# Performance work log

Measured on AMD Instinct MI355X. Metric: run time of the kernel, lower is better.

## Reference

```python
import jax, jax.numpy as jnp
import numpy as np

D = 1024
H = 4
HD = D // H
B = 256
L = 64
DILATIONS = (1, 4, 8, 16)


def setup_inputs() -> dict:
    key = jax.random.key(0)
    ks = jax.random.split(key, 12)
    s = 1.0 / np.sqrt(D)
    return {
        "x": jax.random.normal(ks[0], (B, D), jnp.float32),
        "hist": jax.random.normal(ks[1], (L, B, D), jnp.float32),
        "Wq": jax.random.normal(ks[2], (D, D), jnp.float32) * s,
        "bq": jnp.zeros((D,), jnp.float32),
        "Wk": jax.random.normal(ks[3], (D, D), jnp.float32) * s,
        "bk": jnp.zeros((D,), jnp.float32),
        "Wv": jax.random.normal(ks[4], (D, D), jnp.float32) * s,
        "bv": jnp.zeros((D,), jnp.float32),
        "Wo": jax.random.normal(ks[5], (D, D), jnp.float32) * s,
        "bo": jnp.zeros((D,), jnp.float32),
        "dil_w": jnp.full((len(DILATIONS),), 1.0 / len(DILATIONS), jnp.float32),
        "gamma": jnp.ones((D,), jnp.float32),
        "beta": jnp.zeros((D,), jnp.float32),
    }


def reference(x, hist, Wq, bq, Wk, bk, Wv, bv, Wo, bo, dil_w, gamma, beta):
    scale = 1.0 / np.sqrt(HD)
    q = (x @ Wq + bq).reshape(B, H, HD)  # (B, H, HD)
    attended = []
    for d in DILATIONS:
        # history frames at stride d, concatenated along dim 0 (faithful to torch.cat)
        frames = hist[::d].reshape(-1, D)              # (T', D), T' = ceil(L/d)*B
        k = (frames @ Wk + bk).reshape(-1, H, HD)      # (T', H, HD)
        v = (frames @ Wv + bv).reshape(-1, H, HD)
        s = jnp.einsum('bhd,thd->bht', q, k) * scale   # (B, H, T')
        a = jax.nn.softmax(s, axis=-1)
        attended.append(jnp.einsum('bht,thd->bhd', a, v).reshape(B, D))
    w = jax.nn.softmax(dil_w, axis=0)
    combined = sum(w[i] * attended[i] for i in range(len(DILATIONS)))
    y = x + combined @ Wo + bo
    mu = jnp.mean(y, axis=-1, keepdims=True)
    var = jnp.var(y, axis=-1, keepdims=True)
    return (y - mu) / jnp.sqrt(var + 1e-5) * gamma + beta
```

## Files before the change

kernel.cpp:

```cpp
#include <hip/hip_runtime.h>


#define DD    1024
#define TALL  16384

typedef _Float16 half8  __attribute__((ext_vector_type(8)));
typedef _Float16 half4v __attribute__((ext_vector_type(4)));
typedef float    floatx4 __attribute__((ext_vector_type(4)));
typedef unsigned int u32;

static const size_t OFF_WOT  = 0;
static const size_t OFF_WV16 = 2097152;
static const size_t OFF_WK16 = 4194304;
static const size_t OFF_WQ16 = 6291456;
static const size_t OFF_XB   = 8388608;
static const size_t OFF_G    = 8912896;
static const size_t OFF_WVOT = 11010048;
static const size_t OFF_WQKT = 19398656;
static const size_t OFF_BVWO = 27787264;
static const size_t OFF_BQK  = 27791360;
static const size_t OFF_PHR  = 27807744;
static const size_t OFF_OPP  = 29904896;
static const size_t OFF_HB   = 38293504;
static const size_t OFF_PHP  = OFF_HB;
static const size_t OFF_HT   = 71848960;
static const size_t OFF_S    = 105403392;

__device__ __forceinline__ void gl_lds16(const void* g, void* l) {
  __builtin_amdgcn_global_load_lds((const __attribute__((address_space(1))) u32*)g,
                                   (__attribute__((address_space(3))) u32*)l, 16, 0, 0);
}

__global__ void prep_kernel(const float* __restrict__ Wo, const float* __restrict__ Wv,
                            const float* __restrict__ Wk, const float* __restrict__ Wq,
                            const float* __restrict__ x, const float* __restrict__ hist,
                            _Float16* __restrict__ WoT, _Float16* __restrict__ Wv16,
                            _Float16* __restrict__ Wk16, _Float16* __restrict__ Wq16,
                            _Float16* __restrict__ xb, _Float16* __restrict__ histb,
                            _Float16* __restrict__ histT) {
  int bid = blockIdx.x, tid = threadIdx.x;
  if (bid < 1024) {
    int k0 = (bid & 31) * 32, n0 = (bid >> 5) * 32;
    __shared__ float t32[32][33];
    int tx = tid & 31, ty = tid >> 5;
#pragma unroll
    for (int i = 0; i < 4; i++) {
      int r = ty + i * 8;
      t32[r][tx] = Wo[(size_t)(k0 + r) * DD + n0 + tx];
    }
    __syncthreads();
#pragma unroll
    for (int i = 0; i < 4; i++) {
      int r = ty + i * 8;
      WoT[(size_t)(n0 + r) * DD + k0 + tx] = (_Float16)t32[tx][r];
    }
  } else if (bid < 4352) {
    const float* src; _Float16* dst; size_t i;
    if (bid < 2048)      { src = Wv; dst = Wv16; i = (size_t)(bid - 1024) * 256 + tid; }
    else if (bid < 3072) { src = Wk; dst = Wk16; i = (size_t)(bid - 2048) * 256 + tid; }
    else if (bid < 4096) { src = Wq; dst = Wq16; i = (size_t)(bid - 3072) * 256 + tid; }
    else                 { src = x;  dst = xb;   i = (size_t)(bid - 4096) * 256 + tid; }
    float4 v = ((const float4*)src)[i];
    half4v h = {(_Float16)v.x, (_Float16)v.y, (_Float16)v.z, (_Float16)v.w};
    *(half4v*)(dst + 4 * i) = h;
  } else {
    int tb = bid - 4352;
    int t0 = (tb & 255) * 64, f0 = (tb >> 8) * 64;
    __shared__ _Float16 lt[64][72];
    int r = tid >> 2, c0 = (tid & 3) * 16;
    half8 s0, s1;
#pragma unroll
    for (int i = 0; i < 4; i++) {
      float4 v = *(const float4*)&hist[(size_t)(t0 + r) * 1024 + f0 + c0 + i * 4];
      half4v h = {(_Float16)v.x, (_Float16)v.y, (_Float16)v.z, (_Float16)v.w};
      *(half4v*)&lt[r][c0 + i * 4] = h;
      if (i < 2) { s0[i*4]=h[0]; s0[i*4+1]=h[1]; s0[i*4+2]=h[2]; s0[i*4+3]=h[3]; }
      else { s1[(i-2)*4]=h[0]; s1[(i-2)*4+1]=h[1]; s1[(i-2)*4+2]=h[2]; s1[(i-2)*4+3]=h[3]; }
    }
    *(half8*)&histb[(size_t)(t0 + r) * 1024 + f0 + c0] = s0;
    *(half8*)&histb[(size_t)(t0 + r) * 1024 + f0 + c0 + 8] = s1;
    __syncthreads();
    int fr = tid >> 2, tc0 = (tid & 3) * 16;
    half8 o0, o1;
#pragma unroll
    for (int j = 0; j < 8; j++) { o0[j] = lt[tc0 + j][fr]; o1[j] = lt[tc0 + 8 + j][fr]; }
    *(half8*)&histT[(size_t)(f0 + fr) * TALL + t0 + tc0] = o0;
    *(half8*)&histT[(size_t)(f0 + fr) * TALL + t0 + tc0 + 8] = o1;
  }
}

__device__ __forceinline__ void gemm_core(const _Float16* __restrict__ A, size_t lda,
                                          const _Float16* __restrict__ B, size_t ldb,
                                          int kIters, _Float16* As, _Float16* Bs,
                                          int tid, floatx4 acc[4][4]) {
  int lane = tid & 63, w = tid >> 6;
  int l15 = lane & 15, quad = lane >> 4;
  int wm = (w >> 1) * 64, wn = (w & 1) * 64;
  int swz = ((tid & 3) ^ ((tid >> 3) & 3)) * 8;
  int pch = (quad ^ ((l15 >> 1) & 3)) * 8;
  const char* gA0 = (const char*)(A + (size_t)(tid >> 2) * lda + swz);
  const char* gA1 = (const char*)(A + ((size_t)(tid >> 2) + 64) * lda + swz);
  const char* gB0 = (const char*)(B + (size_t)(tid >> 2) * ldb + swz);
  const char* gB1 = (const char*)(B + ((size_t)(tid >> 2) + 64) * ldb + swz);
  _Float16* lA0 = As + w * 512; _Float16* lA1 = As + 2048 + w * 512;
  _Float16* lB0 = Bs + w * 512; _Float16* lB1 = Bs + 2048 + w * 512;
  for (int kk = 0; kk < kIters; kk++) {
    __syncthreads();
    size_t off = (size_t)kk * 64;
    gl_lds16(gA0 + off, lA0);
    gl_lds16(gA1 + off, lA1);
    gl_lds16(gB0 + off, lB0);
    gl_lds16(gB1 + off, lB1);
    __syncthreads();
    half8 a[4];
#pragma unroll
    for (int mi = 0; mi < 4; mi++) a[mi] = *(const half8*)&As[(wm + mi * 16 + l15) * 32 + pch];
#pragma unroll
    for (int ni = 0; ni < 4; ni++) {
      half8 b8 = *(const half8*)&Bs[(wn + ni * 16 + l15) * 32 + pch];
#pragma unroll
      for (int mi = 0; mi < 4; mi++)
        acc[mi][ni] = __builtin_amdgcn_mfma_f32_16x16x32_f16(a[mi], b8, acc[mi][ni], 0, 0, 0);
    }
  }
}

template <bool OUTF32>
__launch_bounds__(256, 3)
__global__ void gemm_f16_kernel(const _Float16* __restrict__ A, size_t lda, size_t aoffz,
                                const _Float16* __restrict__ B, size_t ldb, size_t boffz,
                                int kIters, const float* __restrict__ bias, size_t biasoffz,
                                float scale, void* __restrict__ C, size_t ldc, size_t coffz) {
  __shared__ __align__(16) _Float16 As[4096];
  __shared__ __align__(16) _Float16 Bs[4096];
  int tid = threadIdx.x;
  const _Float16* Ab = A + aoffz * blockIdx.z + (size_t)(blockIdx.y * 128) * lda;
  const _Float16* Bb = B + boffz * blockIdx.z + (size_t)(blockIdx.x * 128) * ldb;
  floatx4 acc[4][4];
  floatx4 zero = {0.f, 0.f, 0.f, 0.f};
#pragma unroll
  for (int a = 0; a < 4; a++)
#pragma unroll
    for (int b = 0; b < 4; b++) acc[a][b] = zero;
  gemm_core(Ab, lda, Bb, ldb, kIters, As, Bs, tid, acc);
  int lane = tid & 63, w = tid >> 6;
  int l15 = lane & 15, quad = lane >> 4;
  int wm = (w >> 1) * 64, wn = (w & 1) * 64;
#pragma unroll
  for (int mi = 0; mi < 4; mi++)
#pragma unroll
    for (int ni = 0; ni < 4; ni++) {
      int colg = blockIdx.x * 128 + wn + ni * 16 + l15;
      float bv = bias ? bias[biasoffz * blockIdx.z + colg] : 0.f;
#pragma unroll
      for (int r = 0; r < 4; r++) {
        int rowg = blockIdx.y * 128 + wm + mi * 16 + quad * 4 + r;
        float v = (acc[mi][ni][r] + bv) * scale;
        size_t idx = coffz * blockIdx.z + (size_t)rowg * ldc + colg;
        if (OUTF32) ((float*)C)[idx] = v;
        else ((_Float16*)C)[idx] = (_Float16)v;
      }
    }
}

__launch_bounds__(256, 3)
__global__ void wpack_kernel(const _Float16* __restrict__ WoT, const _Float16* __restrict__ Wv16,
                             const _Float16* __restrict__ Wk16, const _Float16* __restrict__ Wq16,
                             const float* __restrict__ bv, const float* __restrict__ bq,
                             _Float16* __restrict__ WVOT, _Float16* __restrict__ WQKT,
                             float* __restrict__ bvwo, float* __restrict__ bqk) {
  __shared__ __align__(16) _Float16 As[4096];
  __shared__ __align__(16) _Float16 Bs[4096];
  int bid = blockIdx.x, tid = threadIdx.x;
  if (bid < 512) {
    bool isQK = bid >= 256;
    int g = bid & 255;
    int x = g & 7, y = (g >> 3) & 7, z = g >> 6;
    const _Float16* A = isQK ? Wk16 : WoT;
    const _Float16* B = isQK ? Wq16 : Wv16;
    const _Float16* Ab = A + 256 * z + (size_t)(y * 128) * 1024;
    const _Float16* Bb = B + 256 * z + (size_t)(x * 128) * 1024;
    floatx4 acc[4][4];
    floatx4 zero = {0.f, 0.f, 0.f, 0.f};
#pragma unroll
    for (int a = 0; a < 4; a++)
#pragma unroll
      for (int b = 0; b < 4; b++) acc[a][b] = zero;
    gemm_core(Ab, 1024, Bb, 1024, 8, As, Bs, tid, acc);
    float scale = isQK ? 0.0625f : 1.0f;
    _Float16* C = isQK ? WQKT : WVOT;
    size_t ldc = isQK ? 1024 : 4096;
    size_t zoff = isQK ? (size_t)1048576 * z : (size_t)1024 * z;
    int lane = tid & 63, w = tid >> 6;
    int l15 = lane & 15, quad = lane >> 4;
    int wm = (w >> 1) * 64, wn = (w & 1) * 64;
#pragma unroll
    for (int mi = 0; mi < 4; mi++)
#pragma unroll
      for (int ni = 0; ni < 4; ni++) {
        int col = x * 128 + wn + ni * 16 + l15;
#pragma unroll
        for (int r = 0; r < 4; r++) {
          int row = y * 128 + wm + mi * 16 + quad * 4 + r;
          C[zoff + (size_t)row * ldc + col] = (_Float16)(acc[mi][ni][r] * scale);
        }
      }
  } else if (bid < 516) {
    int j = (bid - 512) * 256 + tid;
    const half8* row = (const half8*)(WoT + (size_t)j * 1024);
    float a = 0.f;
    for (int c = 0; c < 128; c++) {
      half8 w8 = row[c];
#pragma unroll
      for (int e = 0; e < 8; e++) a += bv[c * 8 + e] * (float)w8[e];
    }
    bvwo[j] = a;
  } else {
    int idx = (bid - 516) * 256 + tid;
    int h = idx >> 10, f = idx & 1023;
    const _Float16* row = Wk16 + (size_t)f * 1024 + h * 256;
    float a = 0.f;
    for (int n = 0; n < 256; n++) a += bq[h * 256 + n] * (float)row[n];
    bqk[idx] = a * 0.0625f;
  }
}

__launch_bounds__(256, 3)
__global__ void gemm_s_kernel(const _Float16* __restrict__ G, const _Float16* __restrict__ histb,
                              _Float16* __restrict__ S) {
  __shared__ __align__(16) _Float16 As[4096];
  __shared__ __align__(16) _Float16 Bs[4096];
  int bid = blockIdx.x, tid = threadIdx.x;
  int b7 = bid & 7, rr = bid >> 3;
  int x = ((rr & 15) << 3) | b7;
  int yh = rr >> 4;
  int y = yh & 1, h = yh >> 1;
  const _Float16* Ab = G + (size_t)h * 262144 + (size_t)(y * 128) * 1024;
  const _Float16* Bb = histb + (size_t)(x * 128) * 1024;
  floatx4 acc[4][4];
  floatx4 zero = {0.f, 0.f, 0.f, 0.f};
#pragma unroll
  for (int a = 0; a < 4; a++)
#pragma unroll
    for (int b = 0; b < 4; b++) acc[a][b] = zero;
  gemm_core(Ab, 1024, Bb, 1024, 32, As, Bs, tid, acc);
  int lane = tid & 63, w = tid >> 6;
  int l15 = lane & 15, quad = lane >> 4;
  int wm = (w >> 1) * 64, wn = (w & 1) * 64;
#pragma unroll
  for (int mi = 0; mi < 4; mi++)
#pragma unroll
    for (int ni = 0; ni < 4; ni++) {
      int col = x * 128 + wn + ni * 16 + l15;
#pragma unroll
      for (int r = 0; r < 4; r++) {
        int row = y * 128 + wm + mi * 16 + quad * 4 + r;
        S[(size_t)h * 4194304 + (size_t)row * TALL + col] = (_Float16)acc[mi][ni][r];
      }
    }
}

__global__ void softmax_kernel(_Float16* __restrict__ S, const float* __restrict__ dil_w) {
  int r = blockIdx.x, tid = threadIdx.x;
  _Float16* row = S + (size_t)r * TALL;
  int lane = tid & 63;
  float ef[8][8];
  float es[8];
  __shared__ float Zf[64];
  __shared__ float Zd[4];
  __shared__ float cf[64];
#pragma unroll
  for (int i = 0; i < 8; i++) {
    half8 v = *(const half8*)&row[((size_t)i * 256 + tid) * 8];
    float s = 0.f;
#pragma unroll
    for (int j = 0; j < 8; j++) { float e = __expf((float)v[j]); ef[i][j] = e; s += e; }
#pragma unroll
    for (int off = 1; off <= 16; off <<= 1) s += __shfl_xor(s, off, 64);
    es[i] = s;
  }
  if ((lane & 31) == 0) {
    int half = tid >> 5;
#pragma unroll
    for (int i = 0; i < 8; i++) Zf[i * 8 + half] = es[i];
  }
  __syncthreads();
  if (tid < 4) {
    int step = 1 << (tid + (tid ? 1 : 0));
    float z = 0.f;
    for (int f = 0; f < 64; f += step) z += Zf[f];
    Zd[tid] = z;
  }
  __syncthreads();
  if (tid < 64) {
    float w0 = dil_w[0], w1 = dil_w[1], w2 = dil_w[2], w3 = dil_w[3];
    float wmx = fmaxf(fmaxf(w0, w1), fmaxf(w2, w3));
    float e0 = __expf(w0 - wmx), e1 = __expf(w1 - wmx), e2 = __expf(w2 - wmx), e3 = __expf(w3 - wmx);
    float wsum = e0 + e1 + e2 + e3;
    float c = (e0 / wsum) / Zd[0];
    if ((tid & 3) == 0) c += (e1 / wsum) / Zd[1];
    if ((tid & 7) == 0) c += (e2 / wsum) / Zd[2];
    if ((tid & 15) == 0) c += (e3 / wsum) / Zd[3];
    cf[tid] = c * 256.0f;
  }
  __syncthreads();
#pragma unroll
  for (int i = 0; i < 8; i++) {
    float c = cf[i * 8 + (tid >> 5)];
    half8 o;
#pragma unroll
    for (int j = 0; j < 8; j++) o[j] = (_Float16)(ef[i][j] * c);
    *(half8*)&row[((size_t)i * 256 + tid) * 8] = o;
  }
}

__launch_bounds__(256, 3)
__global__ void gemm_ph_kernel(const _Float16* __restrict__ P, const _Float16* __restrict__ histT,
                               float* __restrict__ part) {
  __shared__ __align__(16) _Float16 As[4096];
  __shared__ __align__(16) _Float16 Bs[4096];
  int bid = blockIdx.x, tid = threadIdx.x;
  int sp = bid & 7, rr = bid >> 3;
  int x = rr & 7, yh = rr >> 3;
  int y = yh & 1, h = yh >> 1;
  const _Float16* Ab = P + (size_t)h * 4194304 + (size_t)(y * 128) * TALL + sp * 2048;
  const _Float16* Bb = histT + (size_t)(x * 128) * TALL + sp * 2048;
  floatx4 acc[4][4];
  floatx4 zero = {0.f, 0.f, 0.f, 0.f};
#pragma unroll
  for (int a = 0; a < 4; a++)
#pragma unroll
    for (int b = 0; b < 4; b++) acc[a][b] = zero;
  gemm_core(Ab, TALL, Bb, TALL, 64, As, Bs, tid, acc);
  int lane = tid & 63, w = tid >> 6;
  int l15 = lane & 15, quad = lane >> 4;
  int wm = (w >> 1) * 64, wn = (w & 1) * 64;
#pragma unroll
  for (int mi = 0; mi < 4; mi++)
#pragma unroll
    for (int ni = 0; ni < 4; ni++) {
      int k = x * 128 + wn + ni * 16 + l15;
#pragma unroll
      for (int r = 0; r < 4; r++) {
        int q = y * 128 + wm + mi * 16 + quad * 4 + r;
        part[(size_t)(h * 8 + sp) * 262144 + (size_t)q * 1024 + k] = acc[mi][ni][r];
      }
    }
}

__global__ void reduce_ph_kernel(const float* __restrict__ part, _Float16* __restrict__ PHred) {
  size_t e4 = ((size_t)blockIdx.x * 256 + threadIdx.x) * 4;
  int q = (int)(e4 >> 12);
  int hk = (int)(e4 & 4095);
  int h = hk >> 10, k = hk & 1023;
  float4 s = {0.f, 0.f, 0.f, 0.f};
#pragma unroll
  for (int sp = 0; sp < 8; sp++) {
    float4 p = *(const float4*)&part[(size_t)(h * 8 + sp) * 262144 + (size_t)q * 1024 + k];
    s.x += p.x; s.y += p.y; s.z += p.z; s.w += p.w;
  }
  half4v o = {(_Float16)s.x, (_Float16)s.y, (_Float16)s.z, (_Float16)s.w};
  *(half4v*)&PHred[e4] = o;
}

__global__ void ln_kernel(const float* __restrict__ x, const float* __restrict__ part2,
                          const float* __restrict__ bo, const float* __restrict__ bvwo,
                          const float* __restrict__ gamma, const float* __restrict__ beta,
                          float* __restrict__ out) {
  int b = blockIdx.x, t = threadIdx.x;
  __shared__ float red[8];
  float y[4];
  float sum = 0.f, sq = 0.f;
#pragma unroll
  for (int i = 0; i < 4; i++) {
    int j = t + i * 256;
    float v = x[(size_t)b * 1024 + j] + bo[j] + bvwo[j];
#pragma unroll
    for (int z = 0; z < 8; z++) v += part2[(size_t)z * 262144 + (size_t)b * 1024 + j];
    y[i] = v;
    sum += v;
    sq += v * v;
  }
#pragma unroll
  for (int off = 1; off < 64; off <<= 1) {
    sum += __shfl_xor(sum, off, 64);
    sq += __shfl_xor(sq, off, 64);
  }
  int w = t >> 6, lane = t & 63;
  if (lane == 0) { red[w] = sum; red[4 + w] = sq; }
  __syncthreads();
  sum = red[0] + red[1] + red[2] + red[3];
  sq = red[4] + red[5] + red[6] + red[7];
  float mu = sum * (1.f / 1024.f);
  float var = sq * (1.f / 1024.f) - mu * mu;
  float inv = rsqrtf(var + 1e-5f);
#pragma unroll
  for (int i = 0; i < 4; i++) {
    int j = t + i * 256;
    out[(size_t)b * 1024 + j] = (y[i] - mu) * inv * gamma[j] + beta[j];
  }
}

extern "C" void kernel_launch(void* const* d_in, const int* in_sizes, int n_in,
                              void* d_out, int out_size, void* d_ws, size_t ws_size,
                              hipStream_t stream) {
  const float* x     = (const float*)d_in[0];
  const float* hist  = (const float*)d_in[1];
  const float* Wq    = (const float*)d_in[2];
  const float* bq    = (const float*)d_in[3];
  const float* Wk    = (const float*)d_in[4];
  const float* Wv    = (const float*)d_in[6];
  const float* bv    = (const float*)d_in[7];
  const float* Wo    = (const float*)d_in[8];
  const float* bo    = (const float*)d_in[9];
  const float* dil_w = (const float*)d_in[10];
  const float* gamma = (const float*)d_in[11];
  const float* beta  = (const float*)d_in[12];
  char* ws = (char*)d_ws;

  _Float16* WoT   = (_Float16*)(ws + OFF_WOT);
  _Float16* Wv16  = (_Float16*)(ws + OFF_WV16);
  _Float16* Wk16  = (_Float16*)(ws + OFF_WK16);
  _Float16* Wq16  = (_Float16*)(ws + OFF_WQ16);
  _Float16* xb    = (_Float16*)(ws + OFF_XB);
  _Float16* G     = (_Float16*)(ws + OFF_G);
  _Float16* WVOT  = (_Float16*)(ws + OFF_WVOT);
  _Float16* WQKT  = (_Float16*)(ws + OFF_WQKT);
  float* bvwo     = (float*)(ws + OFF_BVWO);
  float* bqk      = (float*)(ws + OFF_BQK);
  _Float16* PHred = (_Float16*)(ws + OFF_PHR);
  float* oppart   = (float*)(ws + OFF_OPP);
  _Float16* histb = (_Float16*)(ws + OFF_HB);
  float* phpart   = (float*)(ws + OFF_PHP);
  _Float16* histT = (_Float16*)(ws + OFF_HT);
  _Float16* Sb    = (_Float16*)(ws + OFF_S);

  prep_kernel<<<dim3(8448), 256, 0, stream>>>(Wo, Wv, Wk, Wq, x, hist,
                                              WoT, Wv16, Wk16, Wq16, xb, histb, histT);
  wpack_kernel<<<dim3(532), 256, 0, stream>>>(WoT, Wv16, Wk16, Wq16, bv, bq,
                                              WVOT, WQKT, bvwo, bqk);
  gemm_f16_kernel<false><<<dim3(8, 2, 4), 256, 0, stream>>>(
      xb, 1024, 0, WQKT, 1024, 1048576, 32, bqk, 1024, 1.0f, (void*)G, 1024, 262144);
  gemm_s_kernel<<<dim3(1024), 256, 0, stream>>>(G, histb, Sb);
  softmax_kernel<<<dim3(1024), 256, 0, stream>>>(Sb, dil_w);
  gemm_ph_kernel<<<dim3(512), 256, 0, stream>>>(Sb, histT, phpart);
  reduce_ph_kernel<<<dim3(1024), 256, 0, stream>>>(phpart, PHred);
  gemm_f16_kernel<true><<<dim3(8, 2, 8), 256, 0, stream>>>(
      PHred, 4096, 512, WVOT, 4096, 512, 16, nullptr, 0, 1.0f / 256.0f,
      (void*)oppart, 1024, 262144);
  ln_kernel<<<dim3(256), 256, 0, stream>>>(x, oppart, bo, bvwo, gamma, beta, (float*)d_out);
}
```

Before: 327.5 us.

## Triple-buffer LDS tiles in shared GEMM core with async prefetch two stages ahead

Replaces the two-barrier load-then-compute loop in gemm_core with a three-stage ring of LDS buffers. Global-to-LDS copies for iteration k+2 are issued while iteration k runs its MFMAs, and progress is tracked with explicit vmcnt waits and a single s_barrier per iteration. The goal is to hide global memory latency behind compute. In exchange, LDS per block triples to 48KB, which may limit occupancy, and correctness now depends on the hand-written waitcnt counts matching the number of outstanding loads.

```diff
diff --git a/kernel.cpp b/kernel.cpp
--- a/kernel.cpp
+++ b/kernel.cpp
@@ -102,27 +102,47 @@
   const char* gA1 = (const char*)(A + ((size_t)(tid >> 2) + 64) * lda + swz);
   const char* gB0 = (const char*)(B + (size_t)(tid >> 2) * ldb + swz);
   const char* gB1 = (const char*)(B + ((size_t)(tid >> 2) + 64) * ldb + swz);
-  _Float16* lA0 = As + w * 512; _Float16* lA1 = As + 2048 + w * 512;
-  _Float16* lB0 = Bs + w * 512; _Float16* lB1 = Bs + 2048 + w * 512;
+  _Float16* lA = As + w * 512;
+  _Float16* lB = Bs + w * 512;
+#define GC_STAGE(buf, k)                                    \
+  do {                                                      \
+    size_t off_ = (size_t)(k) * 64;                         \
+    _Float16* la_ = lA + (buf) * 4096;                      \
+    _Float16* lb_ = lB + (buf) * 4096;                      \
+    gl_lds16(gA0 + off_, la_);                              \
+    gl_lds16(gA1 + off_, la_ + 2048);                       \
+    gl_lds16(gB0 + off_, lb_);                              \
+    gl_lds16(gB1 + off_, lb_ + 2048);                       \
+  } while (0)
+  GC_STAGE(0, 0);
+  if (kIters > 1) GC_STAGE(1, 1);
+  int cur = 0;
   for (int kk = 0; kk < kIters; kk++) {
-    __syncthreads();
-    size_t off = (size_t)kk * 64;
-    gl_lds16(gA0 + off, lA0);
-    gl_lds16(gA1 + off, lA1);
-    gl_lds16(gB0 + off, lB0);
-    gl_lds16(gB1 + off, lB1);
-    __syncthreads();
+    if (kk + 1 < kIters) {
+      asm volatile("s_waitcnt vmcnt(4)" ::: "memory");
+    } else {
+      asm volatile("s_waitcnt vmcnt(0)" ::: "memory");
+    }
+    asm volatile("s_barrier" ::: "memory");
+    if (kk + 2 < kIters) {
+      int nb = cur + 2; if (nb >= 3) nb -= 3;
+      GC_STAGE(nb, kk + 2);
+    }
+    const _Float16* Ac = As + cur * 4096;
+    const _Float16* Bc = Bs + cur * 4096;
     half8 a[4];
 #pragma unroll
-    for (int mi = 0; mi < 4; mi++) a[mi] = *(const half8*)&As[(wm + mi * 16 + l15) * 32 + pch];
+    for (int mi = 0; mi < 4; mi++) a[mi] = *(const half8*)&Ac[(wm + mi * 16 + l15) * 32 + pch];
 #pragma unroll
     for (int ni = 0; ni < 4; ni++) {
-      half8 b8 = *(const half8*)&Bs[(wn + ni * 16 + l15) * 32 + pch];
+      half8 b8 = *(const half8*)&Bc[(wn + ni * 16 + l15) * 32 + pch];
 #pragma unroll
       for (int mi = 0; mi < 4; mi++)
         acc[mi][ni] = __builtin_amdgcn_mfma_f32_16x16x32_f16(a[mi], b8, acc[mi][ni], 0, 0, 0);
     }
-  }
+    cur++; if (cur >= 3) cur = 0;
+  }
+#undef GC_STAGE
 }
 
 template <bool OUTF32>
@@ -131,8 +151,8 @@
                                 const _Float16* __restrict__ B, size_t ldb, size_t boffz,
                                 int kIters, const float* __restrict__ bias, size_t biasoffz,
                                 float scale, void* __restrict__ C, size_t ldc, size_t coffz) {
-  __shared__ __align__(16) _Float16 As[4096];
-  __shared__ __align__(16) _Float16 Bs[4096];
+  __shared__ __align__(16) _Float16 As[12288];
+  __shared__ __align__(16) _Float16 Bs[12288];
   int tid = threadIdx.x;
   const _Float16* Ab = A + aoffz * blockIdx.z + (size_t)(blockIdx.y * 128) * lda;
   const _Float16* Bb = B + boffz * blockIdx.z + (size_t)(blockIdx.x * 128) * ldb;
@@ -169,8 +189,8 @@
                              const float* __restrict__ bv, const float* __restrict__ bq,
                              _Float16* __restrict__ WVOT, _Float16* __restrict__ WQKT,
                              float* __restrict__ bvwo, float* __restrict__ bqk) {
-  __shared__ __align__(16) _Float16 As[4096];
-  __shared__ __align__(16) _Float16 Bs[4096];
+  __shared__ __align__(16) _Float16 As[12288];
+  __shared__ __align__(16) _Float16 Bs[12288];
   int bid = blockIdx.x, tid = threadIdx.x;
   if (bid < 512) {
     bool isQK = bid >= 256;
@@ -228,8 +248,8 @@
 __launch_bounds__(256, 3)
 __global__ void gemm_s_kernel(const _Float16* __restrict__ G, const _Float16* __restrict__ histb,
                               _Float16* __restrict__ S) {
-  __shared__ __align__(16) _Float16 As[4096];
-  __shared__ __align__(16) _Float16 Bs[4096];
+  __shared__ __align__(16) _Float16 As[12288];
+  __shared__ __align__(16) _Float16 Bs[12288];
   int bid = blockIdx.x, tid = threadIdx.x;
   int b7 = bid & 7, rr = bid >> 3;
   int x = ((rr & 15) << 3) | b7;
@@ -317,8 +337,8 @@
 __launch_bounds__(256, 3)
 __global__ void gemm_ph_kernel(const _Float16* __restrict__ P, const _Float16* __restrict__ histT,
                                float* __restrict__ part) {
-  __shared__ __align__(16) _Float16 As[4096];
-  __shared__ __align__(16) _Float16 Bs[4096];
+  __shared__ __align__(16) _Float16 As[12288];
+  __shared__ __align__(16) _Float16 Bs[12288];
   int bid = blockIdx.x, tid = threadIdx.x;
   int sp = bid & 7, rr = bid >> 3;
   int x = rr & 7, yh = rr >> 3;
```

Measured after the change: 340.1 us. 3.8% more time.

## Double-buffer LDS in shared GEMM core to overlap global loads with MFMA

Applied to the files above, without the earlier changes.

Rewrites the shared GEMM inner loop to use two LDS buffers, prefetching tile k+2 while computing tile k. Explicit vmcnt waits and raw barriers replace the two __syncthreads per iteration. All GEMM kernels get doubled shared memory arrays, and gemm_s's launch bound is raised to 4 blocks per CU. It targets the global-load latency stall, at the cost of more LDS per block, which may reduce occupancy. The unroll by two assumes kIters is even.

```diff
diff --git a/kernel.cpp b/kernel.cpp
--- a/kernel.cpp
+++ b/kernel.cpp
@@ -102,27 +102,47 @@
   const char* gA1 = (const char*)(A + ((size_t)(tid >> 2) + 64) * lda + swz);
   const char* gB0 = (const char*)(B + (size_t)(tid >> 2) * ldb + swz);
   const char* gB1 = (const char*)(B + ((size_t)(tid >> 2) + 64) * ldb + swz);
-  _Float16* lA0 = As + w * 512; _Float16* lA1 = As + 2048 + w * 512;
-  _Float16* lB0 = Bs + w * 512; _Float16* lB1 = Bs + 2048 + w * 512;
-  for (int kk = 0; kk < kIters; kk++) {
-    __syncthreads();
-    size_t off = (size_t)kk * 64;
-    gl_lds16(gA0 + off, lA0);
-    gl_lds16(gA1 + off, lA1);
-    gl_lds16(gB0 + off, lB0);
-    gl_lds16(gB1 + off, lB1);
-    __syncthreads();
-    half8 a[4];
-#pragma unroll
-    for (int mi = 0; mi < 4; mi++) a[mi] = *(const half8*)&As[(wm + mi * 16 + l15) * 32 + pch];
-#pragma unroll
-    for (int ni = 0; ni < 4; ni++) {
-      half8 b8 = *(const half8*)&Bs[(wn + ni * 16 + l15) * 32 + pch];
-#pragma unroll
-      for (int mi = 0; mi < 4; mi++)
-        acc[mi][ni] = __builtin_amdgcn_mfma_f32_16x16x32_f16(a[mi], b8, acc[mi][ni], 0, 0, 0);
-    }
-  }
+  _Float16* lA = As + w * 512;
+  _Float16* lB = Bs + w * 512;
+#define GC_STAGE(buf, k)                                    \
+  do {                                                      \
+    size_t off_ = (size_t)(k) * 64;                         \
+    gl_lds16(gA0 + off_, lA + (buf) * 4096);                \
+    gl_lds16(gA1 + off_, lA + (buf) * 4096 + 2048);         \
+    gl_lds16(gB0 + off_, lB + (buf) * 4096);                \
+    gl_lds16(gB1 + off_, lB + (buf) * 4096 + 2048);         \
+  } while (0)
+#define GC_STEP(buf, k)                                                       \
+  do {                                                                        \
+    if ((k) + 1 < kIters) asm volatile("s_waitcnt vmcnt(4)" ::: "memory");    \
+    else                  asm volatile("s_waitcnt vmcnt(0)" ::: "memory");    \
+    asm volatile("s_barrier" ::: "memory");                                   \
+    const _Float16* Ac_ = As + (buf) * 4096;                                  \
+    const _Float16* Bc_ = Bs + (buf) * 4096;                                  \
+    half8 a_[4];                                                              \
+    _Pragma("unroll")                                                         \
+    for (int mi = 0; mi < 4; mi++)                                            \
+      a_[mi] = *(const half8*)&Ac_[(wm + mi * 16 + l15) * 32 + pch];          \
+    _Pragma("unroll")                                                         \
+    for (int ni = 0; ni < 4; ni++) {                                          \
+      half8 b8_ = *(const half8*)&Bc_[(wn + ni * 16 + l15) * 32 + pch];       \
+      _Pragma("unroll")                                                       \
+      for (int mi = 0; mi < 4; mi++)                                          \
+        acc[mi][ni] = __builtin_amdgcn_mfma_f32_16x16x32_f16(a_[mi], b8_,     \
+                                                             acc[mi][ni], 0, 0, 0); \
+    }                                                                         \
+    asm volatile("s_waitcnt lgkmcnt(0)" ::: "memory");                        \
+    asm volatile("s_barrier" ::: "memory");                                   \
+    if ((k) + 2 < kIters) GC_STAGE(buf, (k) + 2);                             \
+  } while (0)
+  GC_STAGE(0, 0);
+  GC_STAGE(1, 1);
+  for (int kk = 0; kk < kIters; kk += 2) {
+    GC_STEP(0, kk);
+    GC_STEP(1, kk + 1);
+  }
+#undef GC_STEP
+#undef GC_STAGE
 }
 
 template <bool OUTF32>
@@ -131,8 +151,8 @@
                                 const _Float16* __restrict__ B, size_t ldb, size_t boffz,
                                 int kIters, const float* __restrict__ bias, size_t biasoffz,
                                 float scale, void* __restrict__ C, size_t ldc, size_t coffz) {
-  __shared__ __align__(16) _Float16 As[4096];
-  __shared__ __align__(16) _Float16 Bs[4096];
+  __shared__ __align__(16) _Float16 As[8192];
+  __shared__ __align__(16) _Float16 Bs[8192];
   int tid = threadIdx.x;
   const _Float16* Ab = A + aoffz * blockIdx.z + (size_t)(blockIdx.y * 128) * lda;
   const _Float16* Bb = B + boffz * blockIdx.z + (size_t)(blockIdx.x * 128) * ldb;
@@ -169,8 +189,8 @@
                              const float* __restrict__ bv, const float* __restrict__ bq,
                              _Float16* __restrict__ WVOT, _Float16* __restrict__ WQKT,
                              float* __restrict__ bvwo, float* __restrict__ bqk) {
-  __shared__ __align__(16) _Float16 As[4096];
-  __shared__ __align__(16) _Float16 Bs[4096];
+  __shared__ __align__(16) _Float16 As[8192];
+  __shared__ __align__(16) _Float16 Bs[8192];
   int bid = blockIdx.x, tid = threadIdx.x;
   if (bid < 512) {
     bool isQK = bid >= 256;
@@ -225,11 +245,11 @@
   }
 }
 
-__launch_bounds__(256, 3)
+__launch_bounds__(256, 4)
 __global__ void gemm_s_kernel(const _Float16* __restrict__ G, const _Float16* __restrict__ histb,
                               _Float16* __restrict__ S) {
-  __shared__ __align__(16) _Float16 As[4096];
-  __shared__ __align__(16) _Float16 Bs[4096];
+  __shared__ __align__(16) _Float16 As[8192];
+  __shared__ __align__(16) _Float16 Bs[8192];
   int bid = blockIdx.x, tid = threadIdx.x;
   int b7 = bid & 7, rr = bid >> 3;
   int x = ((rr & 15) << 3) | b7;
@@ -317,8 +337,8 @@
 __launch_bounds__(256, 3)
 __global__ void gemm_ph_kernel(const _Float16* __restrict__ P, const _Float16* __restrict__ histT,
                                float* __restrict__ part) {
-  __shared__ __align__(16) _Float16 As[4096];
-  __shared__ __align__(16) _Float16 Bs[4096];
+  __shared__ __align__(16) _Float16 As[8192];
+  __shared__ __align__(16) _Float16 Bs[8192];
   int bid = blockIdx.x, tid = threadIdx.x;
   int sp = bid & 7, rr = bid >> 3;
   int x = rr & 7, yh = rr >> 3;
```

Result: no change. 323.2 us (-1.3%).
